# Performance work log

Hardware: AMD Instinct MI355X
Metric: run time of the kernel (lower is better)

Reference implementation:

```python
import jax, jax.numpy as jnp
import numpy as np

# Constants hardcoded in SpikingNN.__init__
T, DT = 50.0, 0.125
PREF, PMIN, PTH = 0.0, -1.0, 25.0
D, PSPIKE, TREF = 0.25, 4.0, 5.0
TIME = jnp.asarray(np.arange(0, T + DT, DT), dtype=jnp.float32)  # [401]


def setup_inputs() -> dict:
    key = jax.random.key(0)
    k1, k2 = jax.random.split(key)
    N, L = 131072, TIME.shape[0]  # 131072 traces x 401 timesteps
    S = jax.random.uniform(k1, (N, L), dtype=jnp.float32)
    Pn = jax.random.normal(k2, (N, L), dtype=jnp.float32)  # never read before write; shape only
    return {"Pn": Pn, "S": S}


def _forward(S):
    # S: [N, L]; sequential LIF scan over time, vectorized over N traces.
    t0 = TIME[0]
    P0 = S[:, 0] - D                       # i == 0 branch
    spike0 = P0 >= PTH
    P0 = jnp.where(spike0, P0 + PSPIKE, P0)
    t_rest0 = jnp.where(spike0, t0 + TREF, jnp.zeros_like(P0))  # self.t_rest starts at 0

    def step(carry, xs):
        P_prev, t_rest = carry
        s, t = xs
        # refractory: clamp to Pref; else integrate if above Pmin, else reset to 0
        P = jnp.where(t <= t_rest, PREF,
                      jnp.where(P_prev > PMIN, P_prev + s - D, 0.0))
        spike = P >= PTH
        P = jnp.where(spike, P + PSPIKE, P)        # spike overshoot marker
        t_rest = jnp.where(spike, t + TREF, t_rest)  # enter refractory period
        return (P, t_rest), P

    # scan over time axis: xs are ([L-1, N] currents, [L-1] times)
    (_, _), Ps = jax.lax.scan(step, (P0, t_rest0), (S[:, 1:].T, TIME[1:]))
    return jnp.concatenate([P0[:, None], Ps.T], axis=1)  # [N, L]


def reference(Pn, S):
    # Pn is overwritten in-place in the original before any element is read.
    return _forward(S)
```

## Files before the change

kernel.cpp:

```cpp
#include <hip/hip_runtime.h>


#define N_TRACES 131072
#define L_STEPS  401
#define BLK      256
#define CHUNK    32
#define LDS_PITCH (CHUNK + 1)

__global__ __launch_bounds__(BLK) void snn_scan_kernel(
    const float* __restrict__ S, float* __restrict__ out)
{
    __shared__ float tile[BLK * LDS_PITCH];

    const int tid  = threadIdx.x;
    const int base = blockIdx.x * BLK;
    const int rowS = base * L_STEPS;

    float P      = 0.0f;
    float t_rest = 0.0f;

    for (int c0 = 0; c0 < L_STEPS; c0 += CHUNK) {
        const int ncol = min(CHUNK, L_STEPS - c0);

        #pragma unroll
        for (int k = 0; k < CHUNK; ++k) {
            const int idx = k * BLK + tid;
            const int row = idx >> 5;
            const int col = idx & (CHUNK - 1);
            if (col < ncol) {
                tile[row * LDS_PITCH + col] = S[rowS + row * L_STEPS + c0 + col];
            }
        }
        __syncthreads();

        float* myrow = &tile[tid * LDS_PITCH];
        for (int j = 0; j < ncol; ++j) {
            const int   i = c0 + j;
            const float t = (float)i * 0.125f;
            const float s = myrow[j];
            float p;
            if (i == 0) {
                p = s - 0.25f;
            } else {
                p = (t <= t_rest) ? 0.0f
                                  : ((P > -1.0f) ? ((P + s) - 0.25f) : 0.0f);
            }
            if (p >= 25.0f) {
                p += 4.0f;
                t_rest = t + 5.0f;
            }
            myrow[j] = p;
            P = p;
        }
        __syncthreads();

        #pragma unroll
        for (int k = 0; k < CHUNK; ++k) {
            const int idx = k * BLK + tid;
            const int row = idx >> 5;
            const int col = idx & (CHUNK - 1);
            if (col < ncol) {
                out[rowS + row * L_STEPS + c0 + col] = tile[row * LDS_PITCH + col];
            }
        }
        __syncthreads();
    }
}

extern "C" void kernel_launch(void* const* d_in, const int* in_sizes, int n_in,
                              void* d_out, int out_size, void* d_ws, size_t ws_size,
                              hipStream_t stream)
{
    const float* S   = (const float*)d_in[1];
    float*       out = (float*)d_out;

    const int blocks = N_TRACES / BLK;
    snn_scan_kernel<<<blocks, BLK, 0, stream>>>(S, out);
}
```

Measured before the change: 530.4 us.

## Double-buffer LDS tiles per wave with XOR swizzle and register prefetch

Each wave now stages only its own 64 rows through LDS, so the block-wide __syncthreads barriers are gone. The next chunk is prefetched into registers while the current chunk is scanned. The padded LDS layout is replaced by an XOR swizzle and the per-step loop is fully unrolled with register arrays. The i==0 special case is dropped by starting t_rest at -1. The cost is higher register pressure from the prefetch and scan arrays and doubled shared memory, which may lower occupancy.

```diff
diff --git a/kernel.cpp b/kernel.cpp
--- a/kernel.cpp
+++ b/kernel.cpp
@@ -1,69 +1,103 @@
 #include <hip/hip_runtime.h>
 
 
-#define N_TRACES 131072
-#define L_STEPS  401
-#define BLK      256
-#define CHUNK    32
-#define LDS_PITCH (CHUNK + 1)
+#define NT    131072
+#define L     401
+#define BLKT  256
+#define CHUNK 32
+#define NCH   13
 
-__global__ __launch_bounds__(BLK) void snn_scan_kernel(
+__global__ __launch_bounds__(BLKT) void snn_scan_kernel(
     const float* __restrict__ S, float* __restrict__ out)
 {
-    __shared__ float tile[BLK * LDS_PITCH];
+    __shared__ float smem[2][BLKT * CHUNK];
 
     const int tid  = threadIdx.x;
-    const int base = blockIdx.x * BLK;
-    const int rowS = base * L_STEPS;
+    const int lane = tid & 63;
+    const int wave = tid >> 6;
+    const int l5   = lane >> 5;
+    const int c5   = lane & 31;
+    const int tkey = tid & 31;
 
-    float P      = 0.0f;
-    float t_rest = 0.0f;
+    const int rowBase = blockIdx.x * BLKT;
+    const int wRow    = wave * 64;
 
-    for (int c0 = 0; c0 < L_STEPS; c0 += CHUNK) {
-        const int ncol = min(CHUNK, L_STEPS - c0);
+    {
+        float pre[CHUNK];
+        #pragma unroll
+        for (int k = 0; k < CHUNK; ++k) {
+            const int riw = 2 * k + l5;
+            pre[k] = S[(rowBase + wRow + riw) * L + c5];
+        }
+        #pragma unroll
+        for (int k = 0; k < CHUNK; ++k) {
+            const int riw = 2 * k + l5;
+            smem[0][(wRow + riw) * CHUNK + (c5 ^ (riw & 31))] = pre[k];
+        }
+    }
+
+    float P = 0.0f, t_rest = -1.0f;
+
+    #pragma unroll 1
+    for (int cc = 0; cc < NCH; ++cc) {
+        const int c0 = cc * CHUNK;
+        float* __restrict__ bcur = smem[cc & 1];
+        float* __restrict__ bnxt = smem[(cc + 1) & 1];
+
+        float pre[CHUNK];
+        const bool have_next = (cc + 1 < NCH);
+        if (have_next) {
+            const int c0n = c0 + CHUNK;
+            #pragma unroll
+            for (int k = 0; k < CHUNK; ++k) {
+                const int riw = 2 * k + l5;
+                pre[k] = (c0n + c5 < L)
+                       ? S[(rowBase + wRow + riw) * L + c0n + c5]
+                       : 0.0f;
+            }
+        }
+        asm volatile("" ::: "memory");
+
+        float s[CHUNK];
+        #pragma unroll
+        for (int j = 0; j < CHUNK; ++j)
+            s[j] = bcur[tid * CHUNK + (j ^ tkey)];
+
+        float r[CHUNK];
+        #pragma unroll
+        for (int j = 0; j < CHUNK; ++j) {
+            const float t = (float)(c0 + j) * 0.125f;
+            float p = (t <= t_rest)
+                    ? 0.0f
+                    : ((P > -1.0f) ? (P + s[j]) - 0.25f : 0.0f);
+            const bool spike = (p >= 25.0f);
+            p      = spike ? p + 4.0f : p;
+            t_rest = spike ? t + 5.0f : t_rest;
+            r[j] = p;
+            P    = p;
+        }
+        #pragma unroll
+        for (int j = 0; j < CHUNK; ++j)
+            bcur[tid * CHUNK + (j ^ tkey)] = r[j];
 
         #pragma unroll
         for (int k = 0; k < CHUNK; ++k) {
-            const int idx = k * BLK + tid;
-            const int row = idx >> 5;
-            const int col = idx & (CHUNK - 1);
-            if (col < ncol) {
-                tile[row * LDS_PITCH + col] = S[rowS + row * L_STEPS + c0 + col];
+            const int riw = 2 * k + l5;
+            const float v = bcur[(wRow + riw) * CHUNK + c5];
+            const int col = c5 ^ (riw & 31);
+            if (c0 + col < L)
+                out[(rowBase + wRow + riw) * L + c0 + col] = v;
+        }
+
+        asm volatile("" ::: "memory");
+
+        if (have_next) {
+            #pragma unroll
+            for (int k = 0; k < CHUNK; ++k) {
+                const int riw = 2 * k + l5;
+                bnxt[(wRow + riw) * CHUNK + (c5 ^ (riw & 31))] = pre[k];
             }
         }
-        __syncthreads();
-
-        float* myrow = &tile[tid * LDS_PITCH];
-        for (int j = 0; j < ncol; ++j) {
-            const int   i = c0 + j;
-            const float t = (float)i * 0.125f;
-            const float s = myrow[j];
-            float p;
-            if (i == 0) {
-                p = s - 0.25f;
-            } else {
-                p = (t <= t_rest) ? 0.0f
-                                  : ((P > -1.0f) ? ((P + s) - 0.25f) : 0.0f);
-            }
-            if (p >= 25.0f) {
-                p += 4.0f;
-                t_rest = t + 5.0f;
-            }
-            myrow[j] = p;
-            P = p;
-        }
-        __syncthreads();
-
-        #pragma unroll
-        for (int k = 0; k < CHUNK; ++k) {
-            const int idx = k * BLK + tid;
-            const int row = idx >> 5;
-            const int col = idx & (CHUNK - 1);
-            if (col < ncol) {
-                out[rowS + row * L_STEPS + c0 + col] = tile[row * LDS_PITCH + col];
-            }
-        }
-        __syncthreads();
     }
 }
 
@@ -74,6 +108,5 @@
     const float* S   = (const float*)d_in[1];
     float*       out = (float*)d_out;
 
-    const int blocks = N_TRACES / BLK;
-    snn_scan_kernel<<<blocks, BLK, 0, stream>>>(S, out);
+    snn_scan_kernel<<<NT / BLKT, BLKT, 0, stream>>>(S, out);
 }
```

New measurement: 529.2 us. Within noise of the previous version (-0.2%).

## Stage whole 32-row windows in LDS with float4 loads and prefetch

Applied to the files above, without the earlier changes.

Each block now loads contiguous 32-trace windows (all 401 steps) into LDS with coalesced float4 reads and prefetches the next window into registers while the current one is processed. Only one 32-thread group scans each window, then the whole block writes it back with float4 stores. This targets uncoalesced strided global access and per-chunk barriers. In exchange it serializes the recurrence across eight windows per block and leaves most threads idle during compute.

```diff
diff --git a/kernel.cpp b/kernel.cpp
--- a/kernel.cpp
+++ b/kernel.cpp
@@ -1,69 +1,109 @@
 #include <hip/hip_runtime.h>
 
 
-#define N_TRACES 131072
-#define L_STEPS  401
-#define BLK      256
-#define CHUNK    32
-#define LDS_PITCH (CHUNK + 1)
+#define L        401
+#define BLKT     256
+#define RW       32
+#define NWIN     (BLKT / RW)
+#define WIN_F4   ((RW * L) / 4)
+#define LD_ROUNDS ((WIN_F4 + BLKT - 1) / BLKT)
 
-__global__ __launch_bounds__(BLK) void snn_scan_kernel(
+__global__ __launch_bounds__(BLKT, 2) void snn_scan_kernel(
     const float* __restrict__ S, float* __restrict__ out)
 {
-    __shared__ float tile[BLK * LDS_PITCH];
+    __shared__ float4 buf4[WIN_F4];
+    float* buf = (float*)buf4;
 
-    const int tid  = threadIdx.x;
-    const int base = blockIdx.x * BLK;
-    const int rowS = base * L_STEPS;
+    const int tid = threadIdx.x;
+    const int ts  = blockIdx.x * BLKT;
 
-    float P      = 0.0f;
-    float t_rest = 0.0f;
+    const float4* __restrict__ S4 = (const float4*)S;
+    float4*       __restrict__ O4 = (float4*)out;
 
-    for (int c0 = 0; c0 < L_STEPS; c0 += CHUNK) {
-        const int ncol = min(CHUNK, L_STEPS - c0);
+    {
+        const int b4 = (ts >> 2) * L;
+        float4 pre[LD_ROUNDS];
+        #pragma unroll
+        for (int k = 0; k < LD_ROUNDS; ++k) {
+            const int idx = k * BLKT + tid;
+            if (idx < WIN_F4) pre[k] = S4[b4 + idx];
+        }
+        #pragma unroll
+        for (int k = 0; k < LD_ROUNDS; ++k) {
+            const int idx = k * BLKT + tid;
+            if (idx < WIN_F4) buf4[idx] = pre[k];
+        }
+    }
 
-        #pragma unroll
-        for (int k = 0; k < CHUNK; ++k) {
-            const int idx = k * BLK + tid;
-            const int row = idx >> 5;
-            const int col = idx & (CHUNK - 1);
-            if (col < ncol) {
-                tile[row * LDS_PITCH + col] = S[rowS + row * L_STEPS + c0 + col];
+    #pragma unroll 1
+    for (int g = 0; g < NWIN; ++g) {
+        __syncthreads();
+
+        float4 pre[LD_ROUNDS];
+        if (g + 1 < NWIN) {
+            const int b4 = ((ts + (g + 1) * RW) >> 2) * L;
+            #pragma unroll
+            for (int k = 0; k < LD_ROUNDS; ++k) {
+                const int idx = k * BLKT + tid;
+                if (idx < WIN_F4) pre[k] = S4[b4 + idx];
             }
         }
+
+        if ((tid >> 5) == g) {
+            const int r = tid & 31;
+            float* __restrict__ row = &buf[r * L];
+            float P = 0.0f, t_rest = -1.0f;
+            #pragma unroll 1
+            for (int ib = 0; ib < 50; ++ib) {
+                float sv[8], ov[8];
+                #pragma unroll
+                for (int j = 0; j < 8; ++j) sv[j] = row[ib * 8 + j];
+                #pragma unroll
+                for (int j = 0; j < 8; ++j) {
+                    const float t = (float)(ib * 8 + j) * 0.125f;
+                    float p = (t <= t_rest)
+                            ? 0.0f
+                            : ((P > -1.0f) ? (P + sv[j]) - 0.25f : 0.0f);
+                    const bool spike = (p >= 25.0f);
+                    t_rest = spike ? t + 5.0f : t_rest;
+                    p      = spike ? p + 4.0f : p;
+                    ov[j] = p;
+                    P     = p;
+                }
+                #pragma unroll
+                for (int j = 0; j < 8; ++j) row[ib * 8 + j] = ov[j];
+            }
+            {
+                const float t  = 50.0f;
+                const float sv = row[400];
+                float p = (t <= t_rest)
+                        ? 0.0f
+                        : ((P > -1.0f) ? (P + sv) - 0.25f : 0.0f);
+                if (p >= 25.0f) p += 4.0f;
+                row[400] = p;
+            }
+        }
+
         __syncthreads();
 
-        float* myrow = &tile[tid * LDS_PITCH];
-        for (int j = 0; j < ncol; ++j) {
-            const int   i = c0 + j;
-            const float t = (float)i * 0.125f;
-            const float s = myrow[j];
-            float p;
-            if (i == 0) {
-                p = s - 0.25f;
-            } else {
-                p = (t <= t_rest) ? 0.0f
-                                  : ((P > -1.0f) ? ((P + s) - 0.25f) : 0.0f);
+        {
+            const int b4 = ((ts + g * RW) >> 2) * L;
+            #pragma unroll
+            for (int k = 0; k < LD_ROUNDS; ++k) {
+                const int idx = k * BLKT + tid;
+                if (idx < WIN_F4) O4[b4 + idx] = buf4[idx];
             }
-            if (p >= 25.0f) {
-                p += 4.0f;
-                t_rest = t + 5.0f;
-            }
-            myrow[j] = p;
-            P = p;
         }
+
         __syncthreads();
 
-        #pragma unroll
-        for (int k = 0; k < CHUNK; ++k) {
-            const int idx = k * BLK + tid;
-            const int row = idx >> 5;
-            const int col = idx & (CHUNK - 1);
-            if (col < ncol) {
-                out[rowS + row * L_STEPS + c0 + col] = tile[row * LDS_PITCH + col];
+        if (g + 1 < NWIN) {
+            #pragma unroll
+            for (int k = 0; k < LD_ROUNDS; ++k) {
+                const int idx = k * BLKT + tid;
+                if (idx < WIN_F4) buf4[idx] = pre[k];
             }
         }
-        __syncthreads();
     }
 }
 
@@ -74,6 +114,5 @@
     const float* S   = (const float*)d_in[1];
     float*       out = (float*)d_out;
 
-    const int blocks = N_TRACES / BLK;
-    snn_scan_kernel<<<blocks, BLK, 0, stream>>>(S, out);
+    snn_scan_kernel<<<(131072 / BLKT), BLKT, 0, stream>>>(S, out);
 }
```

New measurement: 568.0 us. 7.1% more time.
